# Performance work log

Measured on AMD Instinct MI355X. Metric: run time of the kernel, lower is better.

Reference implementation:

```python
import jax, jax.numpy as jnp
import numpy as np

B, T, D, S = 4, 8192, 512, 16

def setup_inputs() -> dict:
    key = jax.random.key(0)
    k1, k2, k3, k4, k5 = jax.random.split(key, 5)
    x = jax.random.normal(k1, (B, T, D), dtype=jnp.float32)
    # splat parameters as in __init__: centers ~ 0.02*randn, log_scales = 0
    centers = jax.random.normal(k2, (S, D), dtype=jnp.float32) * 0.02
    log_scales = jnp.zeros((S,), dtype=jnp.float32)
    # xavier-uniform linear weights (gain = 1/(1+layer_idx*0.1) = 1.0 for layer 0)
    limit = float(np.sqrt(6.0 / (D + D)))
    Wv = jax.random.uniform(k3, (D, D), minval=-limit, maxval=limit, dtype=jnp.float32)
    Wo = jax.random.uniform(k4, (D, D), minval=-limit, maxval=limit, dtype=jnp.float32)
    return {"x": x, "centers": centers, "log_scales": log_scales, "Wv": Wv, "Wo": Wo}

def reference(x, centers, log_scales, Wv, Wo):
    # scales clamped as in EnhancedAdaptiveSplat.get_scale
    scales = jnp.clip(jnp.exp(log_scales), 0.1, 2.0)           # [S]
    v = jnp.einsum('btd,ed->bte', x, Wv)                       # value projection [B,T,D]
    # squared distance token<->splat via expansion (no [B,T,S,D] intermediate)
    x2 = jnp.sum(x * x, axis=-1, keepdims=True)                # [B,T,1]
    c2 = jnp.sum(centers * centers, axis=-1)                   # [S]
    xc = jnp.einsum('btd,sd->bts', x, centers)                 # [B,T,S]
    d2 = x2 + c2 - 2.0 * xc                                    # [B,T,S]
    logits = -0.5 * d2 / (scales * scales)                     # gaussian kernel log-weights
    attn = jax.nn.softmax(logits, axis=-1)                     # normalize over splats [B,T,S]
    # tokens -> splats aggregation, then splats -> tokens distribution
    splat_states = jnp.einsum('bts,btd->bsd', attn, v)         # [B,S,D]
    out = jnp.einsum('bts,bsd->btd', attn, splat_states)       # [B,T,D]
    return jnp.einsum('btd,ed->bte', out, Wo)                  # output projection
```

## Files before the change

kernel.cpp:

```cpp
#include <hip/hip_runtime.h>
#include <math.h>

#define B_ 4
#define T_ 8192
#define D_ 512
#define S_ 16

#define CHUNK 32

#define CPAD 516


__device__ __forceinline__ float dot4(float4 a, float4 b) {
  return a.x * b.x + a.y * b.y + a.z * b.z + a.w * b.w;
}

__global__ __launch_bounds__(256, 4) void attn_ts_k(const float* __restrict__ x,
                                                    const float* __restrict__ centers,
                                                    const float* __restrict__ log_scales,
                                                    float* __restrict__ attn,
                                                    float* __restrict__ ts) {
  __shared__ __align__(16) float c_s[S_ * CPAD];
  __shared__ __align__(16) float a_s[CHUNK][S_];
  const int tid = threadIdx.x;
  const int lane = tid & 63;
  const int w = tid >> 6;
  const int s = lane & 15;
  const int tl = lane >> 4;
  const int b = blockIdx.x >> 8;
  const int t0 = (blockIdx.x & 255) * CHUNK;

#pragma unroll
  for (int j = 0; j < 8; ++j) {
    int idx = j * 256 + tid;
    int row = idx >> 7;
    int col = idx & 127;
    float4 v = ((const float4*)centers)[idx];
    *(float4*)(&c_s[row * CPAD + (col << 2)]) = v;
  }
  __syncthreads();

  float c2 = 0.f;
#pragma unroll 4
  for (int d = 0; d < D_; d += 4) {
    float4 cv = *(const float4*)(&c_s[s * CPAD + d]);
    c2 += dot4(cv, cv);
  }

  const float sc = fminf(fmaxf(__expf(log_scales[s]), 0.1f), 2.0f);
  const float inv2 = 0.5f / (sc * sc);

#pragma unroll 1
  for (int pass = 0; pass < 2; ++pass) {
    const int wtok = (w << 3) + (pass << 2) + tl;
    const float* xrow = x + ((size_t)b * T_ + t0 + wtok) * D_;

    float xc = 0.f, x2 = 0.f;
#pragma unroll 1
    for (int d = 0; d < D_; d += 16) {
      float4 xa = *(const float4*)(xrow + d);
      float4 xb = *(const float4*)(xrow + d + 4);
      float4 xv = *(const float4*)(xrow + d + 8);
      float4 xd = *(const float4*)(xrow + d + 12);
      float4 ca = *(const float4*)(&c_s[s * CPAD + d]);
      float4 cb = *(const float4*)(&c_s[s * CPAD + d + 4]);
      float4 cc = *(const float4*)(&c_s[s * CPAD + d + 8]);
      float4 cd = *(const float4*)(&c_s[s * CPAD + d + 12]);
      xc += dot4(xa, ca) + dot4(xb, cb) + dot4(xv, cc) + dot4(xd, cd);
      x2 += dot4(xa, xa) + dot4(xb, xb) + dot4(xv, xv) + dot4(xd, xd);
    }

    float logit = -(x2 + c2 - 2.f * xc) * inv2;

    float m = logit;
    m = fmaxf(m, __shfl_xor(m, 1, 64));
    m = fmaxf(m, __shfl_xor(m, 2, 64));
    m = fmaxf(m, __shfl_xor(m, 4, 64));
    m = fmaxf(m, __shfl_xor(m, 8, 64));
    float e = __expf(logit - m);
    float sum = e;
    sum += __shfl_xor(sum, 1, 64);
    sum += __shfl_xor(sum, 2, 64);
    sum += __shfl_xor(sum, 4, 64);
    sum += __shfl_xor(sum, 8, 64);
    float a = e / sum;

    attn[((size_t)b * T_ + t0 + wtok) * S_ + s] = a;
    a_s[wtok][s] = a;
  }

  __syncthreads();

  {
    const int d = tid;
    float2 acc[S_];
#pragma unroll
    for (int si = 0; si < S_; ++si) acc[si] = make_float2(0.f, 0.f);

    const float* xb = x + ((size_t)b * T_ + t0) * D_;

#pragma unroll 4
    for (int t = 0; t < CHUNK; ++t) {
      float xv0 = xb[(size_t)t * D_ + d];
      float xv1 = xb[(size_t)t * D_ + d + 256];
      const float4* ap = (const float4*)a_s[t];
      float4 q0 = ap[0], q1 = ap[1], q2 = ap[2], q3 = ap[3];
      float av[S_] = {q0.x, q0.y, q0.z, q0.w, q1.x, q1.y, q1.z, q1.w,
                      q2.x, q2.y, q2.z, q2.w, q3.x, q3.y, q3.z, q3.w};
#pragma unroll
      for (int si = 0; si < S_; ++si) {
        acc[si].x += av[si] * xv0;
        acc[si].y += av[si] * xv1;
      }
    }

    float* tb = ts + (size_t)b * S_ * D_;
#pragma unroll
    for (int si = 0; si < S_; ++si) {
      atomicAdd(tb + si * D_ + d, acc[si].x);
      atomicAdd(tb + si * D_ + d + 256, acc[si].y);
    }
  }
}

__global__ __launch_bounds__(256) void proj_k(const float* __restrict__ in,
                                              const float* __restrict__ W,
                                              float* __restrict__ out) {
  __shared__ float red[4][64];
  const int r = blockIdx.x >> 3;
  const int eb = blockIdx.x & 7;
  const int el = threadIdx.x & 63;
  const int kc = threadIdx.x >> 6;
  const int e = (eb << 6) + el;

  const float4* w4 = (const float4*)(W + (size_t)e * D_ + kc * 128);
  const float4* i4 = (const float4*)(in + (size_t)r * D_ + kc * 128);
  float acc = 0.f;
#pragma unroll
  for (int k = 0; k < 32; ++k) acc += dot4(w4[k], i4[k]);

  red[kc][el] = acc;
  __syncthreads();
  if (kc == 0)
    out[(size_t)r * D_ + e] = red[0][el] + red[1][el] + red[2][el] + red[3][el];
}

#define K4_TOK 64
__global__ __launch_bounds__(256) void out_k(const float* __restrict__ attn,
                                             const float* __restrict__ ss_o,
                                             float* __restrict__ out) {
  const int chunks = T_ / K4_TOK;
  const int b = blockIdx.x / chunks;
  const int t0 = (blockIdx.x % chunks) * K4_TOK;
  const int w = threadIdx.x >> 6;
  const int lane = threadIdx.x & 63;
  const int e0 = (w << 7) + (lane << 1);

  float2 ssf[S_];
  const float* sb = ss_o + (size_t)b * S_ * D_;
#pragma unroll
  for (int s = 0; s < S_; ++s) ssf[s] = *(const float2*)(sb + s * D_ + e0);

  const float4* ab = (const float4*)(attn + ((size_t)b * T_ + t0) * S_);
  float* ob = out + ((size_t)b * T_ + t0) * D_ + e0;

#pragma unroll 4
  for (int t = 0; t < K4_TOK; ++t) {
    float4 a0 = ab[t * 4 + 0], a1 = ab[t * 4 + 1];
    float4 a2 = ab[t * 4 + 2], a3 = ab[t * 4 + 3];
    float av[S_] = {a0.x, a0.y, a0.z, a0.w, a1.x, a1.y, a1.z, a1.w,
                    a2.x, a2.y, a2.z, a2.w, a3.x, a3.y, a3.z, a3.w};
    float2 acc = make_float2(0.f, 0.f);
#pragma unroll
    for (int s = 0; s < S_; ++s) {
      acc.x += av[s] * ssf[s].x;
      acc.y += av[s] * ssf[s].y;
    }
    *(float2*)(ob + (size_t)t * D_) = acc;
  }
}

extern "C" void kernel_launch(void* const* d_in, const int* in_sizes, int n_in,
                              void* d_out, int out_size, void* d_ws, size_t ws_size,
                              hipStream_t stream) {
  const float* x          = (const float*)d_in[0];
  const float* centers    = (const float*)d_in[1];
  const float* log_scales = (const float*)d_in[2];
  const float* Wv         = (const float*)d_in[3];
  const float* Wo         = (const float*)d_in[4];
  float* out = (float*)d_out;

  float* attn = (float*)d_ws;
  float* ts   = attn + (size_t)B_ * T_ * S_;
  float* tmp  = ts + (size_t)B_ * S_ * D_;
  float* ss_o = tmp + (size_t)B_ * S_ * D_;

  hipMemsetAsync(ts, 0, (size_t)B_ * S_ * D_ * sizeof(float), stream);

  attn_ts_k<<<B_ * (T_ / CHUNK), 256, 0, stream>>>(x, centers, log_scales, attn, ts);
  proj_k<<<512, 256, 0, stream>>>(ts, Wv, tmp);
  proj_k<<<512, 256, 0, stream>>>(tmp, Wo, ss_o);
  out_k<<<B_ * (T_ / K4_TOK), 256, 0, stream>>>(attn, ss_o, out);
}
```

Before: 207.6 us.

## Compute token-splat logits with bf16 MFMA and double chunk size

The token-to-center dot products now run on the 16x16x32 bf16 matrix cores instead of scalar FP32 FMAs. Center fragments are held in registers, so the shared-memory copy of the centers is dropped. The chunk size rises from 32 to 64 tokens, which halves the number of atomic adds into the splat accumulator, and occupancy hints drop to 2 blocks per CU. Converting x and the centers to bf16 lowers precision in the logits. The x2 - 2xc + c2 expansion with x2 around 512 may amplify that rounding error in the softmax.

After: 179.5 us. 13.5% less time.

```diff
diff --git a/kernel.cpp b/kernel.cpp
--- a/kernel.cpp
+++ b/kernel.cpp
@@ -1,4 +1,5 @@
 #include <hip/hip_runtime.h>
+#include <hip/hip_bf16.h>
 #include <math.h>
 
 #define B_ 4
@@ -6,100 +7,111 @@
 #define D_ 512
 #define S_ 16
 
-#define CHUNK 32
-
-#define CPAD 516
-
+#define CHUNK 64
+
+
+typedef __attribute__((ext_vector_type(8))) short bf16x8;
+typedef __attribute__((ext_vector_type(4))) float f32x4;
 
 __device__ __forceinline__ float dot4(float4 a, float4 b) {
   return a.x * b.x + a.y * b.y + a.z * b.z + a.w * b.w;
 }
 
-__global__ __launch_bounds__(256, 4) void attn_ts_k(const float* __restrict__ x,
+__device__ __forceinline__ bf16x8 pack8(float4 a, float4 b) {
+  union { __hip_bfloat162 h[4]; bf16x8 v; } u;
+  u.h[0] = __float22bfloat162_rn(make_float2(a.x, a.y));
+  u.h[1] = __float22bfloat162_rn(make_float2(a.z, a.w));
+  u.h[2] = __float22bfloat162_rn(make_float2(b.x, b.y));
+  u.h[3] = __float22bfloat162_rn(make_float2(b.z, b.w));
+  return u.v;
+}
+
+__global__ __launch_bounds__(256, 2) void attn_ts_k(const float* __restrict__ x,
                                                     const float* __restrict__ centers,
                                                     const float* __restrict__ log_scales,
                                                     float* __restrict__ attn,
                                                     float* __restrict__ ts) {
-  __shared__ __align__(16) float c_s[S_ * CPAD];
   __shared__ __align__(16) float a_s[CHUNK][S_];
-  const int tid = threadIdx.x;
-  const int lane = tid & 63;
-  const int w = tid >> 6;
-  const int s = lane & 15;
-  const int tl = lane >> 4;
-  const int b = blockIdx.x >> 8;
-  const int t0 = (blockIdx.x & 255) * CHUNK;
-
-#pragma unroll
-  for (int j = 0; j < 8; ++j) {
-    int idx = j * 256 + tid;
-    int row = idx >> 7;
-    int col = idx & 127;
-    float4 v = ((const float4*)centers)[idx];
-    *(float4*)(&c_s[row * CPAD + (col << 2)]) = v;
+  const int lane = threadIdx.x & 63;
+  const int w = threadIdx.x >> 6;
+  const int g = lane >> 4;
+  const int n = lane & 15;
+  const int b = blockIdx.x >> 7;
+  const int t0 = (blockIdx.x & 127) * CHUNK;
+  const int tw = t0 + (w << 4);
+
+  {
+    bf16x8 cf[16];
+    float c2p = 0.f;
+    const float* crow = centers + n * D_ + (g << 3);
+#pragma unroll
+    for (int st = 0; st < 16; ++st) {
+      float4 c0 = *(const float4*)(crow + st * 32);
+      float4 c1 = *(const float4*)(crow + st * 32 + 4);
+      c2p += dot4(c0, c0) + dot4(c1, c1);
+      cf[st] = pack8(c0, c1);
+    }
+    c2p += __shfl_xor(c2p, 16, 64);
+    c2p += __shfl_xor(c2p, 32, 64);
+
+    const float sc = fminf(fmaxf(__expf(log_scales[n]), 0.1f), 2.0f);
+    const float inv2 = 0.5f / (sc * sc);
+
+    const float* xrow = x + ((size_t)b * T_ + tw + n) * D_ + (g << 3);
+    f32x4 acc = {0.f, 0.f, 0.f, 0.f};
+    float x2p = 0.f;
+#pragma unroll
+    for (int st = 0; st < 16; ++st) {
+      float4 x0 = *(const float4*)(xrow + st * 32);
+      float4 x1 = *(const float4*)(xrow + st * 32 + 4);
+      x2p += dot4(x0, x0) + dot4(x1, x1);
+      acc = __builtin_amdgcn_mfma_f32_16x16x32_bf16(pack8(x0, x1), cf[st], acc,
+                                                    0, 0, 0);
+    }
+    x2p += __shfl_xor(x2p, 16, 64);
+    x2p += __shfl_xor(x2p, 32, 64);
+
+    float lg[4];
+#pragma unroll
+    for (int r = 0; r < 4; ++r) {
+      float x2r = __shfl(x2p, (lane & 48) | ((g << 2) + r), 64);
+      lg[r] = (2.f * acc[r] - x2r - c2p) * inv2;
+    }
+
+    float mx[4] = {lg[0], lg[1], lg[2], lg[3]};
+#pragma unroll
+    for (int dlt = 1; dlt < 16; dlt <<= 1)
+#pragma unroll
+      for (int r = 0; r < 4; ++r) mx[r] = fmaxf(mx[r], __shfl_xor(mx[r], dlt, 64));
+    float ev[4], sm[4];
+#pragma unroll
+    for (int r = 0; r < 4; ++r) { ev[r] = __expf(lg[r] - mx[r]); sm[r] = ev[r]; }
+#pragma unroll
+    for (int dlt = 1; dlt < 16; dlt <<= 1)
+#pragma unroll
+      for (int r = 0; r < 4; ++r) sm[r] += __shfl_xor(sm[r], dlt, 64);
+
+    float* ar = attn + ((size_t)b * T_ + tw) * S_;
+#pragma unroll
+    for (int r = 0; r < 4; ++r) {
+      float av = ev[r] / sm[r];
+      int trow = (g << 2) + r;
+      ar[trow * S_ + n] = av;
+      a_s[(w << 4) + trow][n] = av;
+    }
   }
+
   __syncthreads();
 
-  float c2 = 0.f;
-#pragma unroll 4
-  for (int d = 0; d < D_; d += 4) {
-    float4 cv = *(const float4*)(&c_s[s * CPAD + d]);
-    c2 += dot4(cv, cv);
-  }
-
-  const float sc = fminf(fmaxf(__expf(log_scales[s]), 0.1f), 2.0f);
-  const float inv2 = 0.5f / (sc * sc);
-
-#pragma unroll 1
-  for (int pass = 0; pass < 2; ++pass) {
-    const int wtok = (w << 3) + (pass << 2) + tl;
-    const float* xrow = x + ((size_t)b * T_ + t0 + wtok) * D_;
-
-    float xc = 0.f, x2 = 0.f;
-#pragma unroll 1
-    for (int d = 0; d < D_; d += 16) {
-      float4 xa = *(const float4*)(xrow + d);
-      float4 xb = *(const float4*)(xrow + d + 4);
-      float4 xv = *(const float4*)(xrow + d + 8);
-      float4 xd = *(const float4*)(xrow + d + 12);
-      float4 ca = *(const float4*)(&c_s[s * CPAD + d]);
-      float4 cb = *(const float4*)(&c_s[s * CPAD + d + 4]);
-      float4 cc = *(const float4*)(&c_s[s * CPAD + d + 8]);
-      float4 cd = *(const float4*)(&c_s[s * CPAD + d + 12]);
-      xc += dot4(xa, ca) + dot4(xb, cb) + dot4(xv, cc) + dot4(xd, cd);
-      x2 += dot4(xa, xa) + dot4(xb, xb) + dot4(xv, xv) + dot4(xd, xd);
-    }
-
-    float logit = -(x2 + c2 - 2.f * xc) * inv2;
-
-    float m = logit;
-    m = fmaxf(m, __shfl_xor(m, 1, 64));
-    m = fmaxf(m, __shfl_xor(m, 2, 64));
-    m = fmaxf(m, __shfl_xor(m, 4, 64));
-    m = fmaxf(m, __shfl_xor(m, 8, 64));
-    float e = __expf(logit - m);
-    float sum = e;
-    sum += __shfl_xor(sum, 1, 64);
-    sum += __shfl_xor(sum, 2, 64);
-    sum += __shfl_xor(sum, 4, 64);
-    sum += __shfl_xor(sum, 8, 64);
-    float a = e / sum;
-
-    attn[((size_t)b * T_ + t0 + wtok) * S_ + s] = a;
-    a_s[wtok][s] = a;
-  }
-
-  __syncthreads();
-
   {
-    const int d = tid;
+    const int d = threadIdx.x;
     float2 acc[S_];
 #pragma unroll
     for (int si = 0; si < S_; ++si) acc[si] = make_float2(0.f, 0.f);
 
     const float* xb = x + ((size_t)b * T_ + t0) * D_;
 
-#pragma unroll 4
+#pragma unroll 8
     for (int t = 0; t < CHUNK; ++t) {
       float xv0 = xb[(size_t)t * D_ + d];
       float xv1 = xb[(size_t)t * D_ + d + 256];
```
